# Kernel optimization log

Hardware: AMD Instinct MI355X
Metric: run time of the kernel (lower is better)

The kernel has to match this reference:

```python
import jax, jax.numpy as jnp
import numpy as np

IN_FEATURES = 4096
OUT_FEATURES = 4096
INPUT_SCALE = 0.05
OUTPUT_SCALE = 0.05


def setup_inputs() -> dict:
    key = jax.random.key(0)
    k_x, k_w, k_ws = jax.random.split(key, 3)
    # int8 activations (already quantized upstream in W8A8 pipeline)
    x = jax.random.randint(k_x, (4, 2048, IN_FEATURES), -128, 128, dtype=jnp.int32).astype(jnp.int8)
    # simulate per-tensor absmax quantization of an fp32 weight
    w_fp = jax.random.normal(k_w, (OUT_FEATURES, IN_FEATURES), dtype=jnp.float32) * 0.02
    weight_scale = jnp.max(jnp.abs(w_fp)) / 127.0
    w_int8 = jnp.clip(jnp.round(w_fp / weight_scale), -128, 127).astype(jnp.int8)
    weight = w_int8.T  # stored as [in_features, out_features], matching int8_weight.t()
    a = jnp.array([[INPUT_SCALE / OUTPUT_SCALE]], dtype=jnp.float32)
    b = jnp.reshape(weight_scale.astype(jnp.float32), (1, 1))
    return {"x": x, "weight": weight, "a": a, "b": b}


def reference(x, weight, a, b):
    # round and saturate back to int8 (output dtype == x.dtype == int8).
    x_shape = x.shape
    x2 = x.reshape(-1, x_shape[-1]).astype(jnp.int32)          # [N, D]
    acc = jnp.matmul(x2, weight.astype(jnp.int32))             # [N, O] int32 accum
    scale = (a * b)[0, 0]                                      # alpha = in_scale*w_scale/out_scale
    y = jnp.clip(jnp.round(acc.astype(jnp.float32) * scale), -128.0, 127.0).astype(jnp.int8)
    return y.reshape(*x_shape[:-1], -1)
```

## Files before the change

kernel.cpp:

```cpp
#include <hip/hip_runtime.h>
#include <stdint.h>

typedef __attribute__((ext_vector_type(4))) int int4v;
typedef __attribute__((ext_vector_type(4))) uint32_t uint4v;

#define M_DIM 8192
#define N_DIM 4096
#define K_DIM 4096


__global__ void pack_a_perm(const int* __restrict__ x, uint4v* __restrict__ a8) {
    const int g = blockIdx.x * blockDim.x + threadIdx.x;
    const int w0 = (g & 3) * 4;
    const int chunk = g >> 2;
    const int* base = x + (size_t)chunk * 64;
    int4v L[4];
#pragma unroll
    for (int j = 0; j < 4; ++j) L[j] = *(const int4v*)(base + j * 16 + w0);
    uint4v outv;
#pragma unroll
    for (int wi = 0; wi < 4; ++wi) {
        outv[wi] = (uint32_t)(L[0][wi] & 0xff) | ((uint32_t)(L[1][wi] & 0xff) << 8) |
                   ((uint32_t)(L[2][wi] & 0xff) << 16) | ((uint32_t)(L[3][wi] & 0xff) << 24);
    }
    a8[g] = outv;
}

__global__ void transpose_b_perm(const int* __restrict__ w, int8_t* __restrict__ bt) {
    const int t = threadIdx.x;
    const int kt = blockIdx.y * 64;
    const int n0 = blockIdx.x * 64;
    const int c4 = t & 3;
    const int n = t >> 2;
    const int w0 = c4 * 4;
    const int* col = w + (size_t)kt * N_DIM + n0 + n;
    uint4v outv;
#pragma unroll
    for (int wi = 0; wi < 4; ++wi) {
        uint32_t p = 0;
#pragma unroll
        for (int j = 0; j < 4; ++j) {
            uint32_t b = (uint32_t)(col[(size_t)(w0 + wi + 16 * j) * N_DIM] & 0xff);
            p |= b << (8 * j);
        }
        outv[wi] = p;
    }
    *(uint4v*)&bt[(size_t)(n0 + n) * K_DIM + kt + w0 * 4] = outv;
}

__device__ inline void async16(const void* g, void* l) {
    __builtin_amdgcn_global_load_lds(
        (const __attribute__((address_space(1))) uint32_t*)g,
        (__attribute__((address_space(3))) uint32_t*)l, 16, 0, 0);
}

__global__ void __launch_bounds__(256)
gemm_kernel(const int8_t* __restrict__ A, const int8_t* __restrict__ Bt,
            const float* __restrict__ pa, const float* __restrict__ pb,
            int* __restrict__ out) {
    __shared__ int8_t smem[16384];
    int8_t* As = smem;
    int8_t* Bs = smem + 8192;

    const int t = threadIdx.x;
    const int lane = t & 63;
    const int wave = t >> 6;
    const int m0 = blockIdx.y * 128;
    const int n0 = blockIdx.x * 128;
    const int wm = (wave >> 1) * 64;
    const int wn = (wave & 1) * 64;
    const float scale = pa[0] * pb[0];

    int4v acc[4][4];
    int4v zero = {0, 0, 0, 0};
#pragma unroll
    for (int i = 0; i < 4; ++i)
#pragma unroll
        for (int j = 0; j < 4; ++j) acc[i][j] = zero;

    const int rA = lane >> 2;
    const int cA = (lane & 3) * 16;
    const int koff = (lane >> 4) * 16;
    const int fr = lane & 15;

    for (int kt = 0; kt < K_DIM; kt += 64) {
        __syncthreads();
#pragma unroll
        for (int i = 0; i < 2; ++i) {
            int rb = wave * 16 + i * 64;
            async16(A + (size_t)(m0 + rb + rA) * K_DIM + kt + cA, As + rb * 64);
            async16(Bt + (size_t)(n0 + rb + rA) * K_DIM + kt + cA, Bs + rb * 64);
        }
        __syncthreads();

        int4v af[4], bf[4];
#pragma unroll
        for (int i = 0; i < 4; ++i) {
            af[i] = *(const int4v*)&As[(wm + i * 16 + fr) * 64 + koff];
            bf[i] = *(const int4v*)&Bs[(wn + i * 16 + fr) * 64 + koff];
        }
#pragma unroll
        for (int i = 0; i < 4; ++i)
#pragma unroll
            for (int j = 0; j < 4; ++j)
                acc[i][j] = __builtin_amdgcn_mfma_i32_16x16x64_i8(af[i], bf[j],
                                                                  acc[i][j], 0, 0, 0);
    }

    const int orow = (lane >> 4) * 4;
    const int ocol = lane & 15;
#pragma unroll
    for (int i = 0; i < 4; ++i)
#pragma unroll
        for (int j = 0; j < 4; ++j)
#pragma unroll
            for (int r = 0; r < 4; ++r) {
                float v = (float)acc[i][j][r] * scale;
                v = rintf(v);
                v = fminf(127.f, fmaxf(-128.f, v));
                out[(size_t)(m0 + wm + i * 16 + orow + r) * N_DIM +
                    (n0 + wn + j * 16 + ocol)] = (int)v;
            }
}

extern "C" void kernel_launch(void* const* d_in, const int* in_sizes, int n_in,
                              void* d_out, int out_size, void* d_ws, size_t ws_size,
                              hipStream_t stream) {
    const int* x = (const int*)d_in[0];
    const int* w = (const int*)d_in[1];
    const float* pa = (const float*)d_in[2];
    const float* pb = (const float*)d_in[3];
    int* out = (int*)d_out;

    int8_t* a8 = (int8_t*)d_ws;
    int8_t* bt8 = a8 + (size_t)M_DIM * K_DIM;

    const int nwords_a = M_DIM * K_DIM / 16;
    pack_a_perm<<<nwords_a / 256, 256, 0, stream>>>(x, (uint4v*)a8);
    transpose_b_perm<<<dim3(N_DIM / 64, K_DIM / 64), 256, 0, stream>>>(w, bt8);
    gemm_kernel<<<dim3(N_DIM / 128, M_DIM / 128), 256, 0, stream>>>(a8, bt8, pa, pb, out);
}
```

Baseline: 420.7 us.

## Switch GEMM to 32x32x32 int8 MFMA with K=128 tiles and XOR-swizzled LDS

```diff
diff --git a/kernel.cpp b/kernel.cpp
--- a/kernel.cpp
+++ b/kernel.cpp
@@ -2,6 +2,7 @@
 #include <stdint.h>
 
 typedef __attribute__((ext_vector_type(4))) int int4v;
+typedef __attribute__((ext_vector_type(16))) int int16v;
 typedef __attribute__((ext_vector_type(4))) uint32_t uint4v;
 
 #define M_DIM 8192
@@ -58,9 +59,9 @@
 gemm_kernel(const int8_t* __restrict__ A, const int8_t* __restrict__ Bt,
             const float* __restrict__ pa, const float* __restrict__ pb,
             int* __restrict__ out) {
-    __shared__ int8_t smem[16384];
+    __shared__ int8_t smem[32768];
     int8_t* As = smem;
-    int8_t* Bs = smem + 8192;
+    int8_t* Bs = smem + 16384;
 
     const int t = threadIdx.x;
     const int lane = t & 63;
@@ -71,55 +72,67 @@
     const int wn = (wave & 1) * 64;
     const float scale = pa[0] * pb[0];
 
-    int4v acc[4][4];
-    int4v zero = {0, 0, 0, 0};
+    int16v acc[2][2];
 #pragma unroll
-    for (int i = 0; i < 4; ++i)
+    for (int i = 0; i < 2; ++i)
 #pragma unroll
-        for (int j = 0; j < 4; ++j) acc[i][j] = zero;
+        for (int j = 0; j < 2; ++j)
+#pragma unroll
+            for (int r = 0; r < 16; ++r) acc[i][j][r] = 0;
 
-    const int rA = lane >> 2;
-    const int cA = (lane & 3) * 16;
-    const int koff = (lane >> 4) * 16;
-    const int fr = lane & 15;
+    const int srow = lane >> 3;
+    const int sslot = lane & 7;
 
-    for (int kt = 0; kt < K_DIM; kt += 64) {
+    const int fm0 = wm + (lane & 31);
+    const int fn0 = wn + (lane & 31);
+    const int fg = lane >> 5;
+
+    for (int kt = 0; kt < K_DIM; kt += 128) {
         __syncthreads();
 #pragma unroll
-        for (int i = 0; i < 2; ++i) {
-            int rb = wave * 16 + i * 64;
-            async16(A + (size_t)(m0 + rb + rA) * K_DIM + kt + cA, As + rb * 64);
-            async16(Bt + (size_t)(n0 + rb + rA) * K_DIM + kt + cA, Bs + rb * 64);
+        for (int s = 0; s < 4; ++s) {
+            const int base_row = wave * 8 + s * 32;
+            const int row = base_row + srow;
+            const int cA = (sslot ^ (row & 7)) * 16;
+            async16(A + (size_t)(m0 + row) * K_DIM + kt + cA, As + base_row * 128);
+            async16(Bt + (size_t)(n0 + row) * K_DIM + kt + cA, Bs + base_row * 128);
         }
         __syncthreads();
 
-        int4v af[4], bf[4];
 #pragma unroll
-        for (int i = 0; i < 4; ++i) {
-            af[i] = *(const int4v*)&As[(wm + i * 16 + fr) * 64 + koff];
-            bf[i] = *(const int4v*)&Bs[(wn + i * 16 + fr) * 64 + koff];
+        for (int ks = 0; ks < 4; ++ks) {
+            int4v af[2], bf[2];
+            const int cc = ks * 2 + fg;
+#pragma unroll
+            for (int i = 0; i < 2; ++i) {
+                const int ra = fm0 + i * 32;
+                af[i] = *(const int4v*)&As[ra * 128 + ((cc ^ (ra & 7)) * 16)];
+                const int rb = fn0 + i * 32;
+                bf[i] = *(const int4v*)&Bs[rb * 128 + ((cc ^ (rb & 7)) * 16)];
+            }
+#pragma unroll
+            for (int i = 0; i < 2; ++i)
+#pragma unroll
+                for (int j = 0; j < 2; ++j)
+                    acc[i][j] = __builtin_amdgcn_mfma_i32_32x32x32_i8(af[i], bf[j],
+                                                                       acc[i][j], 0, 0, 0);
         }
-#pragma unroll
-        for (int i = 0; i < 4; ++i)
-#pragma unroll
-            for (int j = 0; j < 4; ++j)
-                acc[i][j] = __builtin_amdgcn_mfma_i32_16x16x64_i8(af[i], bf[j],
-                                                                  acc[i][j], 0, 0, 0);
     }
 
-    const int orow = (lane >> 4) * 4;
-    const int ocol = lane & 15;
+    const int col = lane & 31;
+    const int rbase = (lane >> 5) * 4;
 #pragma unroll
-    for (int i = 0; i < 4; ++i)
+    for (int i = 0; i < 2; ++i)
 #pragma unroll
-        for (int j = 0; j < 4; ++j)
+        for (int j = 0; j < 2; ++j)
 #pragma unroll
-            for (int r = 0; r < 4; ++r) {
+            for (int r = 0; r < 16; ++r) {
+                const int rowf = rbase + (r & 3) + 8 * (r >> 2);
                 float v = (float)acc[i][j][r] * scale;
                 v = rintf(v);
                 v = fminf(127.f, fmaxf(-128.f, v));
-                out[(size_t)(m0 + wm + i * 16 + orow + r) * N_DIM +
-                    (n0 + wn + j * 16 + ocol)] = (int)v;
+                out[(size_t)(m0 + wm + i * 32 + rowf) * N_DIM +
+                    (n0 + wn + j * 32 + col)] = (int)v;
             }
 }
 
```

New measurement: 402.2 us. 4.4% less time.
